# Performance work log

Hardware: AMD Instinct MI355X
Metric: run time of the kernel (lower is better)

The kernel has to match this reference:

```python
import jax, jax.numpy as jnp
import numpy as np

D_MODEL = 1024
H = 16
D_K = D_MODEL // H
NEG = -1.0e9


def setup_inputs() -> dict:
    key = jax.random.key(0)
    ks = jax.random.split(key, 12)
    B, S = 2, 2048
    s = 1.0 / np.sqrt(D_MODEL)
    inp = {
        "q": jax.random.normal(ks[0], (B, S, D_MODEL), jnp.float32),
        "k": jax.random.normal(ks[1], (B, S, D_MODEL), jnp.float32),
        "v": jax.random.normal(ks[2], (B, S, D_MODEL), jnp.float32),
        "mask": jnp.tril(jnp.ones((S, S), jnp.int32))[None, None, :, :],
        "wq": jax.random.normal(ks[3], (D_MODEL, D_MODEL), jnp.float32) * s,
        "bq": jax.random.normal(ks[4], (D_MODEL,), jnp.float32) * s,
        "wk": jax.random.normal(ks[5], (D_MODEL, D_MODEL), jnp.float32) * s,
        "bk": jax.random.normal(ks[6], (D_MODEL,), jnp.float32) * s,
        "wv": jax.random.normal(ks[7], (D_MODEL, D_MODEL), jnp.float32) * s,
        "bv": jax.random.normal(ks[8], (D_MODEL,), jnp.float32) * s,
        "wo": jax.random.normal(ks[9], (D_MODEL, D_MODEL), jnp.float32) * s,
        "bo": jax.random.normal(ks[10], (D_MODEL,), jnp.float32) * s,
    }
    return inp


def _split_heads(x):
    # [B,S,D] -> [B,H,S,d_k]
    B, S, _ = x.shape
    return x.reshape(B, S, H, D_K).transpose(0, 2, 1, 3)


def reference(q, k, v, mask, wq, bq, wk, bk, wv, bv, wo, bo):
    # torch Linear: y = x @ W.T + b
    query = _split_heads(q @ wq.T + bq)
    key = _split_heads(k @ wk.T + bk)
    value = _split_heads(v @ wv.T + bv)
    # scores: [B,H,S,S]
    scores = jnp.einsum("bhqd,bhkd->bhqk", query, key) / jnp.sqrt(
        jnp.asarray(D_K, query.dtype))
    scores = jnp.where(mask == 0, jnp.asarray(NEG, scores.dtype), scores)
    attn = jax.nn.softmax(scores, axis=-1)  # dropout p=0.0 -> identity
    x = jnp.einsum("bhqk,bhkd->bhqd", attn, value)
    B, _, S, _ = x.shape
    x = x.transpose(0, 2, 1, 3).reshape(B, S, D_MODEL)
    return x @ wo.T + bo
```

## Files before the change

### kernel.cpp

```cpp
#include <hip/hip_runtime.h>
#include <hip/hip_bf16.h>
#include <cstdint>
#include <cstddef>

#define BATCH 2
#define SEQ   2048
#define DM    1024
#define NH    16
#define DK    64
#define MROWS (BATCH*SEQ)

typedef __bf16 bf16;
typedef float  f32x4  __attribute__((ext_vector_type(4)));
typedef bf16   bf16x8 __attribute__((ext_vector_type(8)));
typedef bf16   bf16x4 __attribute__((ext_vector_type(4)));

#define MFMA32(a, b, c) __builtin_amdgcn_mfma_f32_16x16x32_bf16(a, b, c, 0, 0, 0)

__device__ __forceinline__ void llds16(const void* gc, void* l) {
    void* g = (void*)gc;
    __builtin_amdgcn_global_load_lds(
        (__attribute__((address_space(1))) uint32_t*)g,
        (__attribute__((address_space(3))) uint32_t*)l,
        16, 0, 0);
}

__global__ __launch_bounds__(256) void k_convert(
    const float* __restrict__ q, const float* __restrict__ k, const float* __restrict__ v,
    const float* __restrict__ wq, const float* __restrict__ wk, const float* __restrict__ wv,
    const float* __restrict__ wo,
    bf16* __restrict__ qb, bf16* __restrict__ kb, bf16* __restrict__ vb,
    bf16* __restrict__ wqb, bf16* __restrict__ wkb, bf16* __restrict__ wvb,
    bf16* __restrict__ wob) {
    long t = (long)blockIdx.x * blockDim.x + threadIdx.x;
    const long NQ = (long)MROWS * DM / 4;
    const long NW = (long)DM * DM / 4;
    const float* src; bf16* dst; long off;
    if (t < NQ)            { src = q;  dst = qb;  off = t; }
    else if (t < 2*NQ)     { src = k;  dst = kb;  off = t - NQ; }
    else if (t < 3*NQ)     { src = v;  dst = vb;  off = t - 2*NQ; }
    else {
        long u = t - 3*NQ;
        if (u < NW)        { src = wq; dst = wqb; off = u; }
        else if (u < 2*NW) { src = wk; dst = wkb; off = u - NW; }
        else if (u < 3*NW) { src = wv; dst = wvb; off = u - 2*NW; }
        else               { src = wo; dst = wob; off = u - 3*NW; }
    }
    f32x4 x = *(const f32x4*)(src + off * 4);
    bf16x4 y;
    y[0] = (bf16)x[0]; y[1] = (bf16)x[1]; y[2] = (bf16)x[2]; y[3] = (bf16)x[3];
    *(bf16x4*)(dst + off * 4) = y;
}

__device__ __forceinline__ void gemm_main(const bf16* __restrict__ A, const bf16* __restrict__ B,
                                          int m0, int n0, f32x4 acc[4][4]) {
    constexpr int K = DM, BK = 32;
    __shared__ bf16 sA[8 * 512];
    __shared__ bf16 sB[8 * 512];
    const int tid = threadIdx.x;
    const int l = tid & 63, w = tid >> 6;
    const int lr = l & 15, lc = l >> 4;
    const int wm = w & 1, wn = w >> 1;

    for (int k0 = 0; k0 < K; k0 += BK) {
#pragma unroll
        for (int i = 0; i < 2; ++i) {
            int e = w * 2 + i;
            const bf16* ga = A + (size_t)(m0 + e * 16 + lr) * K + k0 + lc * 8;
            const bf16* gb = B + (size_t)(n0 + e * 16 + lr) * K + k0 + lc * 8;
            llds16(ga, &sA[e * 512]);
            llds16(gb, &sB[e * 512]);
        }
        __syncthreads();

        bf16x8 af[4], bfr[4];
#pragma unroll
        for (int mi = 0; mi < 4; ++mi)
            af[mi] = *(const bf16x8*)&sA[(size_t)(wm * 4 + mi) * 512 + l * 8];
#pragma unroll
        for (int ni = 0; ni < 4; ++ni)
            bfr[ni] = *(const bf16x8*)&sB[(size_t)(wn * 4 + ni) * 512 + l * 8];
#pragma unroll
        for (int mi = 0; mi < 4; ++mi)
#pragma unroll
            for (int ni = 0; ni < 4; ++ni)
                acc[mi][ni] = MFMA32(af[mi], bfr[ni], acc[mi][ni]);
        __syncthreads();
    }
}

__global__ __launch_bounds__(256) void k_gemm_qkv(
    const bf16* __restrict__ qb, const bf16* __restrict__ kb, const bf16* __restrict__ vb,
    const bf16* __restrict__ wqb, const bf16* __restrict__ wkb, const bf16* __restrict__ wvb,
    const float* __restrict__ bq, const float* __restrict__ bk, const float* __restrict__ bv,
    bf16* __restrict__ Qf, bf16* __restrict__ Kf, bf16* __restrict__ Vf) {
    const int z = blockIdx.z;
    const bf16* A; const bf16* B; const float* bias;
    int m0, n0;
    if (z == 2) {
        A = vb; B = wvb; bias = bv;
        m0 = blockIdx.x * 128;
        n0 = blockIdx.y * 128;
    } else {
        A = z ? wkb : wqb; B = z ? kb : qb; bias = z ? bk : bq;
        m0 = blockIdx.y * 128;
        n0 = blockIdx.x * 128;
    }
    f32x4 acc[4][4] = {};
    gemm_main(A, B, m0, n0, acc);

    const int tid = threadIdx.x, l = tid & 63, w = tid >> 6;
    const int quad = l >> 4, l15 = l & 15;
    const int wm = w & 1, wn = w >> 1;

    if (z == 2) {
#pragma unroll
        for (int ni = 0; ni < 4; ++ni) {
            int dcol = n0 + wn * 64 + ni * 16 + l15;
            int hh2 = dcol >> 6;
            int dtile = (dcol >> 4) & 3;
            float bias_v = bias[dcol];
#pragma unroll
            for (int mi = 0; mi < 4; ++mi) {
                int srow = m0 + wm * 64 + mi * 16;
                int bb = srow >> 11, sl = srow & 2047;
                int kc = sl >> 5;
                int qp = 2 * (mi & 1) + (quad >> 1);
                bf16x4 pack;
#pragma unroll
                for (int r = 0; r < 4; ++r)
                    pack[r] = (bf16)(acc[mi][ni][r] + bias_v);
                size_t entry = ((size_t)(bb * NH + hh2) * 64 + kc) * 4 + dtile;
                *(bf16x4*)(Vf + entry * 512 + (size_t)(qp * 16 + l15) * 8 + (quad & 1) * 4) = pack;
            }
        }
    } else {
        bf16* out = z ? Kf : Qf;
        const float scale = z ? 1.0f : 0.18033688f;
        float bias_rv[4][4];
#pragma unroll
        for (int mi = 0; mi < 4; ++mi)
#pragma unroll
            for (int r = 0; r < 4; ++r)
                bias_rv[mi][r] = bias[m0 + wm * 64 + mi * 16 + quad * 4 + r];
#pragma unroll
        for (int ni = 0; ni < 4; ++ni) {
            int scol = n0 + wn * 64 + ni * 16 + l15;
            int bb = scol >> 11, s = scol & 2047;
            int s16 = s >> 4;
#pragma unroll
            for (int mi = 0; mi < 4; ++mi) {
                int drow = m0 + wm * 64 + mi * 16;
                int hh2 = (drow >> 6) & 15;
                int chunk = (drow & 63) >> 5;
                int qp = 2 * (mi & 1) + (quad >> 1);
                bf16x4 pack;
#pragma unroll
                for (int r = 0; r < 4; ++r)
                    pack[r] = (bf16)((acc[mi][ni][r] + bias_rv[mi][r]) * scale);
                size_t entry = ((size_t)(bb * NH + hh2) * 128 + s16) * 2 + chunk;
                *(bf16x4*)(out + entry * 512 + (size_t)(qp * 16 + l15) * 8 + (quad & 1) * 4) = pack;
            }
        }
    }
}

__global__ __launch_bounds__(256) void k_gemm_out(
    const bf16* __restrict__ X, const bf16* __restrict__ wob,
    const float* __restrict__ bo, float* __restrict__ out) {
    constexpr int K = DM, BK = 32;
    const int m0 = blockIdx.y * 128, n0 = blockIdx.x * 64;
    __shared__ bf16 sA[8 * 512];
    __shared__ bf16 sB[4 * 512];
    const int tid = threadIdx.x;
    const int l = tid & 63, w = tid >> 6;
    const int lr = l & 15, lc = l >> 4;
    const int quad = l >> 4, l15 = l & 15;
    const int wm = w & 1, wn = w >> 1;

    f32x4 acc[4][2] = {};
    for (int k0 = 0; k0 < K; k0 += BK) {
#pragma unroll
        for (int i = 0; i < 2; ++i) {
            int e = w * 2 + i;
            llds16(X + (size_t)(m0 + e * 16 + lr) * K + k0 + lc * 8, &sA[e * 512]);
        }
        llds16(wob + (size_t)(n0 + w * 16 + lr) * K + k0 + lc * 8, &sB[w * 512]);
        __syncthreads();

        bf16x8 af[4], bfr[2];
#pragma unroll
        for (int mi = 0; mi < 4; ++mi)
            af[mi] = *(const bf16x8*)&sA[(size_t)(wm * 4 + mi) * 512 + l * 8];
#pragma unroll
        for (int ni = 0; ni < 2; ++ni)
            bfr[ni] = *(const bf16x8*)&sB[(size_t)(wn * 2 + ni) * 512 + l * 8];
#pragma unroll
        for (int mi = 0; mi < 4; ++mi)
#pragma unroll
            for (int ni = 0; ni < 2; ++ni)
                acc[mi][ni] = MFMA32(af[mi], bfr[ni], acc[mi][ni]);
        __syncthreads();
    }
#pragma unroll
    for (int mi = 0; mi < 4; ++mi)
#pragma unroll
        for (int ni = 0; ni < 2; ++ni) {
            int col = n0 + wn * 32 + ni * 16 + l15;
            float bias_v = bo[col];
            int rbase = m0 + wm * 64 + mi * 16 + quad * 4;
#pragma unroll
            for (int r = 0; r < 4; ++r)
                out[(size_t)(rbase + r) * DM + col] = acc[mi][ni][r] + bias_v;
        }
}

__global__ __launch_bounds__(256, 3) void k_flash(const bf16* __restrict__ Qf,
                                                  const bf16* __restrict__ Kf,
                                                  const bf16* __restrict__ Vf,
                                                  bf16* __restrict__ X) {
    const int bh = blockIdx.x;
    const int qt = 31 - (int)blockIdx.y;
    const int b = bh >> 4, h = bh & 15;
    const int tid = threadIdx.x, w = tid >> 6, l = tid & 63;
    const int quad = l >> 4, l15 = l & 15;
    __shared__ bf16 sKV[2][16 * 512];
    __shared__ bf16 P[4][16 * 72];
    bf16* Pw = P[w];

    const bf16* qfp = Qf + (size_t)bh * 128 * 1024;
    const bf16* kfp = Kf + (size_t)bh * 128 * 1024;
    const bf16* vfp = Vf + (size_t)bh * 64 * 4 * 512;

    const int qt16 = qt * 4 + w;
    const int qglob = qt16 * 16 + l15;

    bf16x8 qf[2];
#pragma unroll
    for (int c = 0; c < 2; ++c)
        qf[c] = *(const bf16x8*)(qfp + ((size_t)qt16 * 2 + c) * 512 + (size_t)l * 8);

    f32x4 o[4] = {};
    float lp = 0.f;

#pragma unroll
    for (int i = 0; i < 4; ++i) {
        int e = w * 4 + i;
        const bf16* src = (e < 8) ? kfp + ((size_t)(0 * 8 + e)) * 512
                                  : vfp + ((size_t)(0 * 8 + (e - 8))) * 512;
        llds16(src + (size_t)l * 8, &sKV[0][e * 512]);
    }

    for (int j = 0; j <= qt; ++j) {
        __syncthreads();
        const bf16* cur = sKV[j & 1];
        if (j < qt) {
            int j1 = j + 1;
#pragma unroll
            for (int i = 0; i < 4; ++i) {
                int e = w * 4 + i;
                const bf16* src = (e < 8) ? kfp + ((size_t)(j1 * 8 + e)) * 512
                                          : vfp + ((size_t)(j1 * 8 + (e - 8))) * 512;
                llds16(src + (size_t)l * 8, (void*)&sKV[j1 & 1][e * 512]);
            }
        }

        f32x4 st[4];
#pragma unroll
        for (int ni = 0; ni < 4; ++ni) {
            bf16x8 k0 = *(const bf16x8*)&cur[(size_t)(ni * 2 + 0) * 512 + l * 8];
            bf16x8 k1 = *(const bf16x8*)&cur[(size_t)(ni * 2 + 1) * 512 + l * 8];
            f32x4 zz = {};
            zz = MFMA32(k0, qf[0], zz);
            st[ni] = MFMA32(k1, qf[1], zz);
        }

        const bool diag = (j == qt);
#pragma unroll
        for (int ni = 0; ni < 4; ++ni) {
            bf16x4 ev;
#pragma unroll
            for (int r = 0; r < 4; ++r) {
                float s = st[ni][r];
                if (diag) {
                    int key = j * 64 + ni * 16 + quad * 4 + r;
                    if (key > qglob) s = -1e30f;
                }
                float e = __builtin_amdgcn_exp2f(s);
                lp += e;
                ev[r] = (bf16)e;
            }
            *(bf16x4*)&Pw[l15 * 72 + ni * 16 + quad * 4] = ev;
        }

#pragma unroll
        for (int c = 0; c < 2; ++c) {
            bf16x8 pb = *(const bf16x8*)&Pw[l15 * 72 + c * 32 + quad * 8];
#pragma unroll
            for (int dt = 0; dt < 4; ++dt) {
                bf16x8 vv = *(const bf16x8*)&cur[(size_t)(8 + c * 4 + dt) * 512 + l * 8];
                o[dt] = MFMA32(vv, pb, o[dt]);
            }
        }
    }

    lp += __shfl_xor(lp, 16, 64);
    lp += __shfl_xor(lp, 32, 64);
    float rv = 1.f / lp;

#pragma unroll
    for (int dt = 0; dt < 4; ++dt) {
        bf16x4 pk;
#pragma unroll
        for (int r = 0; r < 4; ++r)
            pk[r] = (bf16)(o[dt][r] * rv);
        *(bf16x4*)&Pw[l15 * 72 + dt * 16 + quad * 4] = pk;
    }
#pragma unroll
    for (int i = 0; i < 2; ++i) {
        int row = i * 8 + (l >> 3);
        bf16x8 vv = *(const bf16x8*)&Pw[row * 72 + (l & 7) * 8];
        *(bf16x8*)(X + (size_t)(b * SEQ + qt16 * 16 + row) * DM + h * 64 + (l & 7) * 8) = vv;
    }
}

extern "C" void kernel_launch(void* const* d_in, const int* in_sizes, int n_in,
                              void* d_out, int out_size, void* d_ws, size_t ws_size,
                              hipStream_t stream) {
    const float* q  = (const float*)d_in[0];
    const float* k  = (const float*)d_in[1];
    const float* v  = (const float*)d_in[2];
    const float* wq = (const float*)d_in[4];
    const float* bq = (const float*)d_in[5];
    const float* wk = (const float*)d_in[6];
    const float* bk = (const float*)d_in[7];
    const float* wv = (const float*)d_in[8];
    const float* bv = (const float*)d_in[9];
    const float* wo = (const float*)d_in[10];
    const float* bo = (const float*)d_in[11];
    float* out = (float*)d_out;

    uint8_t* ws = (uint8_t*)d_ws;
    const size_t SZ_ACT = (size_t)MROWS * DM * sizeof(bf16);
    const size_t SZ_W   = (size_t)DM * DM * sizeof(bf16);
    bf16* qb  = (bf16*)(ws);
    bf16* kb  = (bf16*)(ws + SZ_ACT);
    bf16* vb  = (bf16*)(ws + 2 * SZ_ACT);
    bf16* wqb = (bf16*)(ws + 3 * SZ_ACT);
    bf16* wkb = (bf16*)(ws + 3 * SZ_ACT + SZ_W);
    bf16* wvb = (bf16*)(ws + 3 * SZ_ACT + 2 * SZ_W);
    bf16* wob = (bf16*)(ws + 3 * SZ_ACT + 3 * SZ_W);
    bf16* Qf  = (bf16*)(ws + 3 * SZ_ACT + 4 * SZ_W);
    bf16* Kf  = (bf16*)(ws + 4 * SZ_ACT + 4 * SZ_W);
    bf16* Vf  = (bf16*)(ws + 5 * SZ_ACT + 4 * SZ_W);
    bf16* X   = (bf16*)(ws + 6 * SZ_ACT + 4 * SZ_W);

    {
        long total_vec4 = 3L * MROWS * DM / 4 + 4L * DM * DM / 4;
        k_convert<<<dim3((unsigned)(total_vec4 / 256)), 256, 0, stream>>>(
            q, k, v, wq, wk, wv, wo, qb, kb, vb, wqb, wkb, wvb, wob);
    }
    k_gemm_qkv<<<dim3(32, 8, 3), 256, 0, stream>>>(
        qb, kb, vb, wqb, wkb, wvb, bq, bk, bv, Qf, Kf, Vf);
    k_flash<<<dim3(BATCH * NH, SEQ / 64), 256, 0, stream>>>(Qf, Kf, Vf, X);
    k_gemm_out<<<dim3(DM / 64, MROWS / 128), 256, 0, stream>>>(X, wob, bo, out);
}
```

Measured before the change: 252.2 us.

## Double-buffer LDS tiles in the projection GEMMs to overlap loads with MFMA

The QKV and output-projection GEMM main loops now use two LDS buffers. The next K-slice is prefetched with global_load_lds while MFMAs run on the current slice, which also drops the second __syncthreads per iteration. The LDS tile layout changes from fragment-blocked to row-major 128x32, so MFMA operand reads now stride 64 bytes across rows and may hit LDS bank conflicts. It also doubles GEMM shared memory use.

```diff
diff --git a/kernel.cpp b/kernel.cpp
--- a/kernel.cpp
+++ b/kernel.cpp
@@ -54,38 +54,47 @@
 
 __device__ __forceinline__ void gemm_main(const bf16* __restrict__ A, const bf16* __restrict__ B,
                                           int m0, int n0, f32x4 acc[4][4]) {
-    constexpr int K = DM, BK = 32;
-    __shared__ bf16 sA[8 * 512];
-    __shared__ bf16 sB[8 * 512];
+    constexpr int K = DM, BK = 32, NS = K / BK;
+    __shared__ bf16 sA[2][128 * BK];
+    __shared__ bf16 sB[2][128 * BK];
     const int tid = threadIdx.x;
     const int l = tid & 63, w = tid >> 6;
-    const int lr = l & 15, lc = l >> 4;
+    const int quad = l >> 4, l15 = l & 15;
     const int wm = w & 1, wn = w >> 1;
-
-    for (int k0 = 0; k0 < K; k0 += BK) {
-#pragma unroll
-        for (int i = 0; i < 2; ++i) {
-            int e = w * 2 + i;
-            const bf16* ga = A + (size_t)(m0 + e * 16 + lr) * K + k0 + lc * 8;
-            const bf16* gb = B + (size_t)(n0 + e * 16 + lr) * K + k0 + lc * 8;
-            llds16(ga, &sA[e * 512]);
-            llds16(gb, &sB[e * 512]);
-        }
+    const int srow = l >> 2, scol = (l & 3) * 8;
+
+#pragma unroll
+    for (int i = 0; i < 2; ++i) {
+        int r16 = w * 32 + i * 16;
+        llds16(A + (size_t)(m0 + r16 + srow) * K + scol, &sA[0][r16 * BK]);
+        llds16(B + (size_t)(n0 + r16 + srow) * K + scol, &sB[0][r16 * BK]);
+    }
+
+    for (int s = 0; s < NS; ++s) {
         __syncthreads();
+        const int cur = s & 1;
+        if (s + 1 < NS) {
+            const int k0 = (s + 1) * BK;
+#pragma unroll
+            for (int i = 0; i < 2; ++i) {
+                int r16 = w * 32 + i * 16;
+                llds16(A + (size_t)(m0 + r16 + srow) * K + k0 + scol, &sA[cur ^ 1][r16 * BK]);
+                llds16(B + (size_t)(n0 + r16 + srow) * K + k0 + scol, &sB[cur ^ 1][r16 * BK]);
+            }
+        }
 
         bf16x8 af[4], bfr[4];
 #pragma unroll
         for (int mi = 0; mi < 4; ++mi)
-            af[mi] = *(const bf16x8*)&sA[(size_t)(wm * 4 + mi) * 512 + l * 8];
+            af[mi] = *(const bf16x8*)&sA[cur][(wm * 64 + mi * 16 + l15) * BK + quad * 8];
 #pragma unroll
         for (int ni = 0; ni < 4; ++ni)
-            bfr[ni] = *(const bf16x8*)&sB[(size_t)(wn * 4 + ni) * 512 + l * 8];
+            bfr[ni] = *(const bf16x8*)&sB[cur][(wn * 64 + ni * 16 + l15) * BK + quad * 8];
 #pragma unroll
         for (int mi = 0; mi < 4; ++mi)
 #pragma unroll
             for (int ni = 0; ni < 4; ++ni)
                 acc[mi][ni] = MFMA32(af[mi], bfr[ni], acc[mi][ni]);
-        __syncthreads();
     }
 }
 
@@ -168,39 +177,49 @@
 __global__ __launch_bounds__(256) void k_gemm_out(
     const bf16* __restrict__ X, const bf16* __restrict__ wob,
     const float* __restrict__ bo, float* __restrict__ out) {
-    constexpr int K = DM, BK = 32;
+    constexpr int K = DM, BK = 32, NS = K / BK;
     const int m0 = blockIdx.y * 128, n0 = blockIdx.x * 64;
-    __shared__ bf16 sA[8 * 512];
-    __shared__ bf16 sB[4 * 512];
+    __shared__ bf16 sA[2][128 * BK];
+    __shared__ bf16 sB[2][64 * BK];
     const int tid = threadIdx.x;
     const int l = tid & 63, w = tid >> 6;
-    const int lr = l & 15, lc = l >> 4;
     const int quad = l >> 4, l15 = l & 15;
     const int wm = w & 1, wn = w >> 1;
+    const int srow = l >> 2, scol = (l & 3) * 8;
+
+#pragma unroll
+    for (int i = 0; i < 2; ++i) {
+        int r16 = w * 32 + i * 16;
+        llds16(X + (size_t)(m0 + r16 + srow) * K + scol, &sA[0][r16 * BK]);
+    }
+    llds16(wob + (size_t)(n0 + w * 16 + srow) * K + scol, &sB[0][w * 16 * BK]);
 
     f32x4 acc[4][2] = {};
-    for (int k0 = 0; k0 < K; k0 += BK) {
-#pragma unroll
-        for (int i = 0; i < 2; ++i) {
-            int e = w * 2 + i;
-            llds16(X + (size_t)(m0 + e * 16 + lr) * K + k0 + lc * 8, &sA[e * 512]);
-        }
-        llds16(wob + (size_t)(n0 + w * 16 + lr) * K + k0 + lc * 8, &sB[w * 512]);
+    for (int s = 0; s < NS; ++s) {
         __syncthreads();
+        const int cur = s & 1;
+        if (s + 1 < NS) {
+            const int k0 = (s + 1) * BK;
+#pragma unroll
+            for (int i = 0; i < 2; ++i) {
+                int r16 = w * 32 + i * 16;
+                llds16(X + (size_t)(m0 + r16 + srow) * K + k0 + scol, &sA[cur ^ 1][r16 * BK]);
+            }
+            llds16(wob + (size_t)(n0 + w * 16 + srow) * K + k0 + scol, &sB[cur ^ 1][w * 16 * BK]);
+        }
 
         bf16x8 af[4], bfr[2];
 #pragma unroll
         for (int mi = 0; mi < 4; ++mi)
-            af[mi] = *(const bf16x8*)&sA[(size_t)(wm * 4 + mi) * 512 + l * 8];
+            af[mi] = *(const bf16x8*)&sA[cur][(wm * 64 + mi * 16 + l15) * BK + quad * 8];
 #pragma unroll
         for (int ni = 0; ni < 2; ++ni)
-            bfr[ni] = *(const bf16x8*)&sB[(size_t)(wn * 2 + ni) * 512 + l * 8];
+            bfr[ni] = *(const bf16x8*)&sB[cur][(wn * 32 + ni * 16 + l15) * BK + quad * 8];
 #pragma unroll
         for (int mi = 0; mi < 4; ++mi)
 #pragma unroll
             for (int ni = 0; ni < 2; ++ni)
                 acc[mi][ni] = MFMA32(af[mi], bfr[ni], acc[mi][ni]);
-        __syncthreads();
     }
 #pragma unroll
     for (int mi = 0; mi < 4; ++mi)
@@ -246,8 +265,8 @@
 #pragma unroll
     for (int i = 0; i < 4; ++i) {
         int e = w * 4 + i;
-        const bf16* src = (e < 8) ? kfp + ((size_t)(0 * 8 + e)) * 512
-                                  : vfp + ((size_t)(0 * 8 + (e - 8))) * 512;
+        const bf16* src = (e < 8) ? kfp + ((size_t)e) * 512
+                                  : vfp + ((size_t)(e - 8)) * 512;
         llds16(src + (size_t)l * 8, &sKV[0][e * 512]);
     }
 
```

New measurement: 235.6 us. 1.07x faster.
